# Optimization experiments

Hardware: AMD Instinct MI355X
Metric: run time of the kernel (lower is better)

Reference implementation:

```python
import jax, jax.numpy as jnp
import numpy as np

B, T, D, H, E, K = 4, 2048, 1024, 2048, 8, 2
LN_EPS = 1e-5


def setup_inputs() -> dict:
    key = jax.random.key(0)
    ks = jax.random.split(key, 5)
    sc = 0.02  # init scale for weights
    return {
        "x": jax.random.normal(ks[0], (B, T, D), dtype=jnp.float32),
        "gate_W": jax.random.normal(ks[1], (D, E), dtype=jnp.float32) * sc,
        "gate_b": jnp.zeros((E,), dtype=jnp.float32),
        "W1": jax.random.normal(ks[2], (E, D, H), dtype=jnp.float32) * sc,
        "b1": jnp.zeros((E, H), dtype=jnp.float32),
        "W2": jax.random.normal(ks[3], (E, H, D), dtype=jnp.float32) * sc,
        "b2": jnp.zeros((E, D), dtype=jnp.float32),
        "ln_gamma": jnp.ones((D,), dtype=jnp.float32),
        "ln_beta": jnp.zeros((D,), dtype=jnp.float32),
    }


def reference(x, gate_W, gate_b, W1, b1, W2, b2, ln_gamma, ln_beta):
    b, t, d = x.shape
    tokens = x.reshape(b * t, d)                      # [N, D]
    n = tokens.shape[0]

    # --- noisy top-k router (eval mode: no noise) ---
    logits = tokens @ gate_W + gate_b                 # [N, E]
    topk_val, topk_idx = jax.lax.top_k(logits, K)     # [N, K]
    topk_prob = jax.nn.softmax(topk_val, axis=-1)
    gates = jnp.zeros_like(logits).at[jnp.arange(n)[:, None], topk_idx].set(topk_prob)  # [N, E]

    # --- experts: dense-equivalent of gather-MLP-scatter (gates are 0 for unselected) ---
    h = jax.nn.gelu(jnp.einsum('nd,edh->enh', tokens, W1) + b1[:, None, :], approximate=False)  # [E,N,H]
    y = jnp.einsum('enh,ehd->end', h, W2) + b2[:, None, :]                                      # [E,N,D]
    out = jnp.einsum('ne,end->nd', gates, y).reshape(b, t, d)

    # --- residual + layernorm ---
    z = out + x
    mu = jnp.mean(z, axis=-1, keepdims=True)
    var = jnp.var(z, axis=-1, keepdims=True)
    out = (z - mu) * jax.lax.rsqrt(var + LN_EPS) * ln_gamma + ln_beta

    # --- aux losses ---
    route_probs = jax.nn.softmax(logits, axis=-1)     # [N, E]
    importance = route_probs.mean(axis=0)             # [E]
    load = (gates > 0).astype(jnp.float32).mean(axis=0)  # [E]
    balance_loss = E * jnp.sum(importance * load)
    eps = 1e-8
    entropy = -(route_probs * jnp.log(route_probs + eps)).sum(axis=-1).mean()
    utilization_entropy = -(load * jnp.log(load + eps)).sum()
    return out, balance_loss, entropy, utilization_entropy, load, importance
```

## Files before the change

kernel.cpp:

```cpp
#include <hip/hip_runtime.h>
#include <math.h>

#define N_TOK 8192
#define DIM   1024
#define HID   2048
#define NE    8
#define NPAIR (N_TOK * 2)
#define CAPP  (NPAIR + NE * 128)
#define TAIL  (N_TOK * DIM)

typedef __bf16 bf16x8_t __attribute__((ext_vector_type(8)));
typedef float  f32x4_t  __attribute__((ext_vector_type(4)));

__device__ __forceinline__ unsigned short f2bf(float f) {
  union { float f; unsigned u; } v; v.f = f;
  unsigned r = v.u + 0x7fffu + ((v.u >> 16) & 1u);
  return (unsigned short)(r >> 16);
}

__device__ __forceinline__ float bf2f(unsigned short h) {
  union { unsigned u; float f; } v; v.u = ((unsigned)h) << 16;
  return v.f;
}

__device__ __forceinline__ float gelu_exact(float v) {
  return 0.5f * v * (1.f + erff(v * 0.70710678118654752440f));
}

__device__ __forceinline__ void load16_lds(const void* g, void* l) {
  __builtin_amdgcn_global_load_lds(
      (const __attribute__((address_space(1))) unsigned int*)g,
      (__attribute__((address_space(3))) unsigned int*)l, 16, 0, 0);
}


template<int KD, int RR>
__global__ __launch_bounds__(256) void w_to_frag(const float* __restrict__ src,
                                                 unsigned short* __restrict__ dst) {
  constexpr int KD32 = KD / 32;
  int z = blockIdx.z;
  int cl = blockIdx.x * 4 + (threadIdx.x >> 6);
  int lane = threadIdx.x & 63, m16 = lane & 15, q = lane >> 4;
  int rblk = cl / KD32, kblk = cl % KD32;
  int r = rblk * 16 + m16;
  int kb = kblk * 32 + q * 8;
  const float* s = src + (size_t)z * KD * RR + (size_t)kb * RR + r;
  unsigned short t[8];
  #pragma unroll
  for (int j = 0; j < 8; ++j) t[j] = f2bf(s[(size_t)j * RR]);
  *(uint4*)(dst + (size_t)z * KD * RR + (size_t)cl * 512 + lane * 8) = *(uint4*)t;
}

#define R_BLOCKS 128
#define R_TPW    (N_TOK / (R_BLOCKS * 4))
__global__ __launch_bounds__(256) void router_kernel(
    const float* __restrict__ x, const float* __restrict__ gW, const float* __restrict__ gb,
    int* __restrict__ tok_e, float* __restrict__ tok_g,
    int* __restrict__ cnt, float* __restrict__ imp, float* __restrict__ ent_sum) {
  __shared__ int s_cnt[NE];
  __shared__ float s_imp[NE];
  __shared__ float s_ent;
  int tid = threadIdx.x;
  if (tid < NE) { s_cnt[tid] = 0; s_imp[tid] = 0.f; }
  if (tid == 0) s_ent = 0.f;
  __syncthreads();
  int wid = tid >> 6, lane = tid & 63;
  int t0 = (blockIdx.x * 4 + wid) * R_TPW;
  float imp_loc[8] = {0.f, 0.f, 0.f, 0.f, 0.f, 0.f, 0.f, 0.f};
  float ent_loc = 0.f;
  for (int t = 0; t < R_TPW; ++t) {
    int n = t0 + t;
    const float* xr = x + (size_t)n * DIM;
    float p[8] = {0.f, 0.f, 0.f, 0.f, 0.f, 0.f, 0.f, 0.f};
    #pragma unroll
    for (int it = 0; it < DIM / 64; ++it) {
      int d = lane + (it << 6);
      float xv = xr[d];
      const float4* g4 = (const float4*)(gW + (size_t)d * NE);
      float4 a = g4[0], b = g4[1];
      p[0] += xv * a.x; p[1] += xv * a.y; p[2] += xv * a.z; p[3] += xv * a.w;
      p[4] += xv * b.x; p[5] += xv * b.y; p[6] += xv * b.z; p[7] += xv * b.w;
    }
    #pragma unroll
    for (int e = 0; e < 8; ++e)
      for (int o = 32; o > 0; o >>= 1) p[e] += __shfl_down(p[e], o, 64);
    if (lane == 0) {
      float lg[8];
      #pragma unroll
      for (int e = 0; e < 8; ++e) lg[e] = p[e] + gb[e];
      int i0 = 0;
      #pragma unroll
      for (int e = 1; e < 8; ++e) if (lg[e] > lg[i0]) i0 = e;
      int i1 = (i0 == 0) ? 1 : 0;
      #pragma unroll
      for (int e = 0; e < 8; ++e) if (e != i0 && lg[e] > lg[i1]) i1 = e;
      float d1 = expf(lg[i1] - lg[i0]);
      float g0 = 1.f / (1.f + d1);
      float g1 = d1 * g0;
      tok_e[2 * n] = i0; tok_e[2 * n + 1] = i1;
      tok_g[2 * n] = g0; tok_g[2 * n + 1] = g1;
      atomicAdd(&s_cnt[i0], 1);
      atomicAdd(&s_cnt[i1], 1);
      float mx = lg[i0], s = 0.f, pe[8];
      #pragma unroll
      for (int e = 0; e < 8; ++e) { pe[e] = expf(lg[e] - mx); s += pe[e]; }
      float inv = 1.f / s;
      #pragma unroll
      for (int e = 0; e < 8; ++e) {
        float pr = pe[e] * inv;
        imp_loc[e] += pr;
        ent_loc -= pr * logf(pr + 1e-8f);
      }
    }
  }
  if (lane == 0) {
    #pragma unroll
    for (int e = 0; e < 8; ++e) atomicAdd(&s_imp[e], imp_loc[e]);
    atomicAdd(&s_ent, ent_loc);
  }
  __syncthreads();
  const float invN = 1.f / (float)N_TOK;
  if (tid < NE) {
    atomicAdd(&cnt[tid], s_cnt[tid]);
    atomicAdd(&imp[tid], s_imp[tid] * invN);
  }
  if (tid == NE) atomicAdd(ent_sum, s_ent * invN);
}

__global__ void finalize_kernel(const int* __restrict__ cnt, int* __restrict__ poffs,
                                int* __restrict__ cursor, const float* __restrict__ imp,
                                const float* __restrict__ ent_sum, float* __restrict__ out_tail) {
  if (threadIdx.x == 0) {
    int off = 0; float bal = 0.f, util = 0.f;
    for (int e = 0; e < NE; ++e) {
      poffs[e] = off; cursor[e] = off;
      off += ((cnt[e] + 127) >> 7) << 7;
      float ld = (float)cnt[e] * (1.f / (float)N_TOK);
      float im = imp[e];
      out_tail[3 + e] = ld;
      out_tail[11 + e] = im;
      bal += im * ld;
      util -= ld * logf(ld + 1e-8f);
    }
    poffs[NE] = off;
    out_tail[0] = (float)NE * bal;
    out_tail[1] = *ent_sum;
    out_tail[2] = util;
  }
}

__global__ __launch_bounds__(256) void scatter_kernel(
    const int* __restrict__ tok_e, const float* __restrict__ tok_g,
    int* __restrict__ cursor, int* __restrict__ row_token, float* __restrict__ row_gate,
    int* __restrict__ pair_slot) {
  __shared__ int s_cnt[NE], s_base[NE], s_rank[NE];
  int tid = threadIdx.x;
  if (tid < NE) { s_cnt[tid] = 0; s_rank[tid] = 0; }
  __syncthreads();
  int n = blockIdx.x * 256 + tid;
  int e0 = tok_e[2 * n], e1 = tok_e[2 * n + 1];
  atomicAdd(&s_cnt[e0], 1);
  atomicAdd(&s_cnt[e1], 1);
  __syncthreads();
  if (tid < NE) s_base[tid] = atomicAdd(&cursor[tid], s_cnt[tid]);
  __syncthreads();
  int r0 = atomicAdd(&s_rank[e0], 1);
  int s0 = s_base[e0] + r0;
  row_token[s0] = n; row_gate[s0] = tok_g[2 * n]; pair_slot[2 * n] = s0;
  int r1 = atomicAdd(&s_rank[e1], 1);
  int s1 = s_base[e1] + r1;
  row_token[s1] = n; row_gate[s1] = tok_g[2 * n + 1]; pair_slot[2 * n + 1] = s1;
}

__global__ __launch_bounds__(256) void gather_a1(
    const float* __restrict__ x, const int* __restrict__ row_token,
    const int* __restrict__ cnt, const int* __restrict__ poffs,
    unsigned short* __restrict__ Ab1) {
  int e = blockIdx.z;
  int base = poffs[e];
  int pcnt = poffs[e + 1] - base;
  int nch = (pcnt >> 4) * 32;
  int cl = blockIdx.x * 4 + (threadIdx.x >> 6);
  if (cl >= nch) return;
  int lane = threadIdx.x & 63, m16 = lane & 15, q = lane >> 4;
  int rblk = cl >> 5, kblk = cl & 31;
  int sl = rblk * 16 + m16;
  int slot = base + sl;
  int tok = (sl < cnt[e]) ? row_token[slot] : 0;
  int k = kblk * 32 + q * 8;
  const float4* sp = (const float4*)(x + (size_t)tok * DIM + k);
  float4 v0 = sp[0], v1 = sp[1];
  unsigned short t[8] = {f2bf(v0.x), f2bf(v0.y), f2bf(v0.z), f2bf(v0.w),
                         f2bf(v1.x), f2bf(v1.y), f2bf(v1.z), f2bf(v1.w)};
  *(uint4*)(Ab1 + ((size_t)(slot >> 4) * 32 + kblk) * 512 + lane * 8) = *(uint4*)t;
}

__global__ __launch_bounds__(256, 4) void expert_gemm1(
    const unsigned short* __restrict__ Ab1,
    const unsigned short* __restrict__ W1f,
    const float* __restrict__ b1,
    const int* __restrict__ poffs,
    unsigned short* __restrict__ He) {
  __shared__ __align__(16) unsigned short As[8192], Bs[8192];
  int e = blockIdx.z;
  int base = poffs[e];
  int pcnt = poffs[e + 1] - base;
  int row0 = blockIdx.x * 128;
  if (row0 >= pcnt) return;
  int col0 = blockIdx.y * 128;
  int tid = threadIdx.x, wid = tid >> 6, lane = tid & 63;
  int m16 = lane & 15, q = lane >> 4;
  int wr = (wid & 1) << 6, wc = (wid >> 1) << 6;
  const unsigned short* Ag = Ab1 + ((size_t)(((base + row0) >> 4) + wid * 2) * 32) * 512 + lane * 8;
  const unsigned short* Bg = W1f + (size_t)e * HID * DIM
                           + ((size_t)((col0 >> 4) + wid * 2) * 32) * 512 + lane * 8;
  unsigned short* lA = As + wid * 4 * 512;
  unsigned short* lB = Bs + wid * 4 * 512;
  f32x4_t zero4 = {0.f, 0.f, 0.f, 0.f};
  f32x4_t acc[4][4];
  #pragma unroll
  for (int i = 0; i < 4; ++i)
    #pragma unroll
    for (int j = 0; j < 4; ++j) acc[i][j] = zero4;
  int ra = wr >> 4, rc = wc >> 4;
  for (int k0 = 0; k0 < DIM; k0 += 64) {
    int kc = (k0 >> 5) * 512;
    load16_lds(Ag + kc,                  lA);
    load16_lds(Ag + kc + 512,            lA + 512);
    load16_lds(Ag + kc + 32 * 512,       lA + 1024);
    load16_lds(Ag + kc + 32 * 512 + 512, lA + 1536);
    load16_lds(Bg + kc,                  lB);
    load16_lds(Bg + kc + 512,            lB + 512);
    load16_lds(Bg + kc + 32 * 512,       lB + 1024);
    load16_lds(Bg + kc + 32 * 512 + 512, lB + 1536);
    __syncthreads();
    #pragma unroll
    for (int ks = 0; ks < 2; ++ks) {
      bf16x8_t a[4], b[4];
      #pragma unroll
      for (int i = 0; i < 4; ++i) {
        a[i] = *(const bf16x8_t*)&As[((ra + i) * 2 + ks) * 512 + lane * 8];
        b[i] = *(const bf16x8_t*)&Bs[((rc + i) * 2 + ks) * 512 + lane * 8];
      }
      #pragma unroll
      for (int i = 0; i < 4; ++i)
        #pragma unroll
        for (int j = 0; j < 4; ++j)
          acc[i][j] = __builtin_amdgcn_mfma_f32_16x16x32_bf16(a[i], b[j], acc[i][j], 0, 0, 0);
    }
    __syncthreads();
  }
  const float* b1e = b1 + (size_t)e * HID;
  int sb = (base + row0) >> 4;
  #pragma unroll
  for (int i = 0; i < 4; ++i) {
    size_t sblk = (size_t)(sb + ra + i);
    #pragma unroll
    for (int rr = 0; rr < 4; ++rr) {
      int s15 = q * 4 + rr;
      #pragma unroll
      for (int j = 0; j < 4; ++j) {
        int col = col0 + wc + j * 16 + m16;
        float v = acc[i][j][rr] + b1e[col];
        size_t off = (sblk * 64 + (col >> 5)) * 512 + (((col >> 3) & 3) * 16 + s15) * 8 + (col & 7);
        He[off] = f2bf(gelu_exact(v));
      }
    }
  }
}

__global__ __launch_bounds__(256, 4) void expert_gemm2(
    const unsigned short* __restrict__ He,
    const unsigned short* __restrict__ W2f,
    const int* __restrict__ poffs,
    unsigned short* __restrict__ yb) {
  __shared__ __align__(16) unsigned short As[8192], Bs[8192];
  int e = blockIdx.z;
  int base = poffs[e];
  int pcnt = poffs[e + 1] - base;
  int row0 = blockIdx.x * 128;
  if (row0 >= pcnt) return;
  int col0 = blockIdx.y * 128;
  int tid = threadIdx.x, wid = tid >> 6, lane = tid & 63;
  int m16 = lane & 15, q = lane >> 4;
  int wr = (wid & 1) << 6, wc = (wid >> 1) << 6;
  const unsigned short* Ag = He + ((size_t)(((base + row0) >> 4) + wid * 2) * 64) * 512 + lane * 8;
  const unsigned short* Bg = W2f + (size_t)e * DIM * HID
                           + ((size_t)((col0 >> 4) + wid * 2) * 64) * 512 + lane * 8;
  unsigned short* lA = As + wid * 4 * 512;
  unsigned short* lB = Bs + wid * 4 * 512;
  f32x4_t zero4 = {0.f, 0.f, 0.f, 0.f};
  f32x4_t acc[4][4];
  #pragma unroll
  for (int i = 0; i < 4; ++i)
    #pragma unroll
    for (int j = 0; j < 4; ++j) acc[i][j] = zero4;
  int ra = wr >> 4, rc = wc >> 4;
  for (int k0 = 0; k0 < HID; k0 += 64) {
    int kc = (k0 >> 5) * 512;
    load16_lds(Ag + kc,                  lA);
    load16_lds(Ag + kc + 512,            lA + 512);
    load16_lds(Ag + kc + 64 * 512,       lA + 1024);
    load16_lds(Ag + kc + 64 * 512 + 512, lA + 1536);
    load16_lds(Bg + kc,                  lB);
    load16_lds(Bg + kc + 512,            lB + 512);
    load16_lds(Bg + kc + 64 * 512,       lB + 1024);
    load16_lds(Bg + kc + 64 * 512 + 512, lB + 1536);
    __syncthreads();
    #pragma unroll
    for (int ks = 0; ks < 2; ++ks) {
      bf16x8_t a[4], b[4];
      #pragma unroll
      for (int i = 0; i < 4; ++i) {
        a[i] = *(const bf16x8_t*)&As[((ra + i) * 2 + ks) * 512 + lane * 8];
        b[i] = *(const bf16x8_t*)&Bs[((rc + i) * 2 + ks) * 512 + lane * 8];
      }
      #pragma unroll
      for (int i = 0; i < 4; ++i)
        #pragma unroll
        for (int j = 0; j < 4; ++j)
          acc[i][j] = __builtin_amdgcn_mfma_f32_16x16x32_bf16(a[i], b[j], acc[i][j], 0, 0, 0);
    }
    __syncthreads();
  }
  #pragma unroll
  for (int i = 0; i < 4; ++i) {
    #pragma unroll
    for (int rr = 0; rr < 4; ++rr) {
      size_t slot = (size_t)(base + row0 + wr + i * 16 + q * 4 + rr);
      #pragma unroll
      for (int j = 0; j < 4; ++j) {
        int col = col0 + wc + j * 16 + m16;
        yb[slot * DIM + col] = f2bf(acc[i][j][rr]);
      }
    }
  }
}

__global__ __launch_bounds__(256) void ln_kernel(
    const float* __restrict__ x, const unsigned short* __restrict__ yb,
    const int* __restrict__ tok_e, const float* __restrict__ tok_g,
    const int* __restrict__ pair_slot, const float* __restrict__ b2,
    const float* __restrict__ gamma, const float* __restrict__ beta,
    float* __restrict__ out) {
  int n = blockIdx.x, tid = threadIdx.x;
  int e0 = tok_e[2 * n], e1 = tok_e[2 * n + 1];
  float g0 = tok_g[2 * n], g1 = tok_g[2 * n + 1];
  size_t s0 = (size_t)pair_slot[2 * n], s1 = (size_t)pair_slot[2 * n + 1];
  const float* xr = x + (size_t)n * DIM;
  const unsigned short* y0 = yb + s0 * DIM;
  const unsigned short* y1 = yb + s1 * DIM;
  const float* b2e0 = b2 + (size_t)e0 * DIM;
  const float* b2e1 = b2 + (size_t)e1 * DIM;
  float z[4], s = 0.f, s2 = 0.f;
  #pragma unroll
  for (int jj = 0; jj < 4; ++jj) {
    int d = tid + (jj << 8);
    float v = xr[d] + g0 * (bf2f(y0[d]) + b2e0[d]) + g1 * (bf2f(y1[d]) + b2e1[d]);
    z[jj] = v; s += v; s2 += v * v;
  }
  for (int o = 32; o > 0; o >>= 1) { s += __shfl_down(s, o, 64); s2 += __shfl_down(s2, o, 64); }
  __shared__ float rs[4], rs2[4];
  int wid = tid >> 6, lane = tid & 63;
  if (lane == 0) { rs[wid] = s; rs2[wid] = s2; }
  __syncthreads();
  float ts = rs[0] + rs[1] + rs[2] + rs[3];
  float ts2 = rs2[0] + rs2[1] + rs2[2] + rs2[3];
  float mu = ts * (1.f / DIM);
  float var = ts2 * (1.f / DIM) - mu * mu;
  float rstd = rsqrtf(var + 1e-5f);
  float* orow = out + (size_t)n * DIM;
  #pragma unroll
  for (int jj = 0; jj < 4; ++jj) {
    int d = tid + (jj << 8);
    orow[d] = (z[jj] - mu) * rstd * gamma[d] + beta[d];
  }
}

extern "C" void kernel_launch(void* const* d_in, const int* in_sizes, int n_in,
                              void* d_out, int out_size, void* d_ws, size_t ws_size,
                              hipStream_t stream) {
  const float* x     = (const float*)d_in[0];
  const float* gW    = (const float*)d_in[1];
  const float* gb    = (const float*)d_in[2];
  const float* W1    = (const float*)d_in[3];
  const float* b1    = (const float*)d_in[4];
  const float* W2    = (const float*)d_in[5];
  const float* b2    = (const float*)d_in[6];
  const float* gamma = (const float*)d_in[7];
  const float* beta  = (const float*)d_in[8];
  float* out = (float*)d_out;

  char* w = (char*)d_ws;
  unsigned short* W1f = (unsigned short*)w; w += (size_t)NE * HID * DIM * 2;
  unsigned short* W2f = (unsigned short*)w; w += (size_t)NE * DIM * HID * 2;
  unsigned short* He  = (unsigned short*)w; w += (size_t)CAPP * HID * 2;
  unsigned short* AbY = (unsigned short*)w; w += (size_t)CAPP * DIM * 2;
  int*   row_token    = (int*)w;            w += (size_t)CAPP * 4;
  float* row_gate     = (float*)w;          w += (size_t)CAPP * 4;
  int*   tok_e        = (int*)w;            w += (size_t)NPAIR * 4;
  float* tok_g        = (float*)w;          w += (size_t)NPAIR * 4;
  int*   pair_slot    = (int*)w;            w += (size_t)NPAIR * 4;
  float* imp          = (float*)w;
  float* ent_sum      = imp + 8;
  int*   cntp         = (int*)(imp + 16);
  int*   cursor       = cntp + 8;
  int*   poffs        = cursor + 8;

  unsigned short* Ab1 = AbY;
  unsigned short* yb  = AbY;

  hipMemsetAsync(imp, 0, 256, stream);

  w_to_frag<DIM, HID><<<dim3(1024, 1, NE), 256, 0, stream>>>(W1, W1f);
  w_to_frag<HID, DIM><<<dim3(1024, 1, NE), 256, 0, stream>>>(W2, W2f);
  router_kernel<<<R_BLOCKS, 256, 0, stream>>>(x, gW, gb, tok_e, tok_g, cntp, imp, ent_sum);
  finalize_kernel<<<1, 64, 0, stream>>>(cntp, poffs, cursor, imp, ent_sum, out + TAIL);
  scatter_kernel<<<N_TOK / 256, 256, 0, stream>>>(tok_e, tok_g, cursor, row_token, row_gate, pair_slot);
  gather_a1<<<dim3(4096, 1, NE), 256, 0, stream>>>(x, row_token, cntp, poffs, Ab1);
  expert_gemm1<<<dim3(64, HID / 128, NE), 256, 0, stream>>>(Ab1, W1f, b1, poffs, He);
  expert_gemm2<<<dim3(64, DIM / 128, NE), 256, 0, stream>>>(He, W2f, poffs, yb);
  ln_kernel<<<N_TOK, 256, 0, stream>>>(x, yb, tok_e, tok_g, pair_slot, b2, gamma, beta, out);
}
```

Before: 529.0 us.

## Double-buffer LDS tiles in both expert GEMMs to overlap loads with MFMA

Both expert GEMM kernels now use two LDS buffers per operand. The loop issues the global-to-LDS load for the next K tile while MFMA runs on the current one, which halves the barriers per tile and hides load latency. The doubled LDS footprint (64 KB per block) forces the launch bound down from 4 to 2 blocks per CU, cutting occupancy and the latency hiding that came from running more blocks at once.

```diff
diff --git a/kernel.cpp b/kernel.cpp
--- a/kernel.cpp
+++ b/kernel.cpp
@@ -195,13 +195,14 @@
   *(uint4*)(Ab1 + ((size_t)(slot >> 4) * 32 + kblk) * 512 + lane * 8) = *(uint4*)t;
 }
 
-__global__ __launch_bounds__(256, 4) void expert_gemm1(
+__global__ __launch_bounds__(256, 2) void expert_gemm1(
     const unsigned short* __restrict__ Ab1,
     const unsigned short* __restrict__ W1f,
     const float* __restrict__ b1,
     const int* __restrict__ poffs,
     unsigned short* __restrict__ He) {
-  __shared__ __align__(16) unsigned short As[8192], Bs[8192];
+  __shared__ __align__(16) unsigned short As0[8192], Bs0[8192];
+  __shared__ __align__(16) unsigned short As1[8192], Bs1[8192];
   int e = blockIdx.z;
   int base = poffs[e];
   int pcnt = poffs[e + 1] - base;
@@ -214,8 +215,6 @@
   const unsigned short* Ag = Ab1 + ((size_t)(((base + row0) >> 4) + wid * 2) * 32) * 512 + lane * 8;
   const unsigned short* Bg = W1f + (size_t)e * HID * DIM
                            + ((size_t)((col0 >> 4) + wid * 2) * 32) * 512 + lane * 8;
-  unsigned short* lA = As + wid * 4 * 512;
-  unsigned short* lB = Bs + wid * 4 * 512;
   f32x4_t zero4 = {0.f, 0.f, 0.f, 0.f};
   f32x4_t acc[4][4];
   #pragma unroll
@@ -223,8 +222,11 @@
     #pragma unroll
     for (int j = 0; j < 4; ++j) acc[i][j] = zero4;
   int ra = wr >> 4, rc = wc >> 4;
-  for (int k0 = 0; k0 < DIM; k0 += 64) {
-    int kc = (k0 >> 5) * 512;
+
+  auto stage = [&](unsigned short* SA, unsigned short* SB, int t) {
+    int kc = t << 10;
+    unsigned short* lA = SA + (wid << 11);
+    unsigned short* lB = SB + (wid << 11);
     load16_lds(Ag + kc,                  lA);
     load16_lds(Ag + kc + 512,            lA + 512);
     load16_lds(Ag + kc + 32 * 512,       lA + 1024);
@@ -233,14 +235,15 @@
     load16_lds(Bg + kc + 512,            lB + 512);
     load16_lds(Bg + kc + 32 * 512,       lB + 1024);
     load16_lds(Bg + kc + 32 * 512 + 512, lB + 1536);
-    __syncthreads();
+  };
+  auto compute = [&](const unsigned short* SA, const unsigned short* SB) {
     #pragma unroll
     for (int ks = 0; ks < 2; ++ks) {
       bf16x8_t a[4], b[4];
       #pragma unroll
       for (int i = 0; i < 4; ++i) {
-        a[i] = *(const bf16x8_t*)&As[((ra + i) * 2 + ks) * 512 + lane * 8];
-        b[i] = *(const bf16x8_t*)&Bs[((rc + i) * 2 + ks) * 512 + lane * 8];
+        a[i] = *(const bf16x8_t*)&SA[((ra + i) * 2 + ks) * 512 + lane * 8];
+        b[i] = *(const bf16x8_t*)&SB[((rc + i) * 2 + ks) * 512 + lane * 8];
       }
       #pragma unroll
       for (int i = 0; i < 4; ++i)
@@ -248,8 +251,20 @@
         for (int j = 0; j < 4; ++j)
           acc[i][j] = __builtin_amdgcn_mfma_f32_16x16x32_bf16(a[i], b[j], acc[i][j], 0, 0, 0);
     }
+  };
+
+  constexpr int NT = DIM / 64;
+  stage(As0, Bs0, 0);
+  __syncthreads();
+  for (int t = 0; t < NT; t += 2) {
+    stage(As1, Bs1, t + 1);
+    compute(As0, Bs0);
     __syncthreads();
-  }
+    if (t + 2 < NT) stage(As0, Bs0, t + 2);
+    compute(As1, Bs1);
+    __syncthreads();
+  }
+
   const float* b1e = b1 + (size_t)e * HID;
   int sb = (base + row0) >> 4;
   #pragma unroll
@@ -269,12 +284,13 @@
   }
 }
 
-__global__ __launch_bounds__(256, 4) void expert_gemm2(
+__global__ __launch_bounds__(256, 2) void expert_gemm2(
     const unsigned short* __restrict__ He,
     const unsigned short* __restrict__ W2f,
     const int* __restrict__ poffs,
     unsigned short* __restrict__ yb) {
-  __shared__ __align__(16) unsigned short As[8192], Bs[8192];
+  __shared__ __align__(16) unsigned short As0[8192], Bs0[8192];
+  __shared__ __align__(16) unsigned short As1[8192], Bs1[8192];
   int e = blockIdx.z;
   int base = poffs[e];
   int pcnt = poffs[e + 1] - base;
@@ -287,8 +303,6 @@
   const unsigned short* Ag = He + ((size_t)(((base + row0) >> 4) + wid * 2) * 64) * 512 + lane * 8;
   const unsigned short* Bg = W2f + (size_t)e * DIM * HID
                            + ((size_t)((col0 >> 4) + wid * 2) * 64) * 512 + lane * 8;
-  unsigned short* lA = As + wid * 4 * 512;
-  unsigned short* lB = Bs + wid * 4 * 512;
   f32x4_t zero4 = {0.f, 0.f, 0.f, 0.f};
   f32x4_t acc[4][4];
   #pragma unroll
@@ -296,8 +310,11 @@
     #pragma unroll
     for (int j = 0; j < 4; ++j) acc[i][j] = zero4;
   int ra = wr >> 4, rc = wc >> 4;
-  for (int k0 = 0; k0 < HID; k0 += 64) {
-    int kc = (k0 >> 5) * 512;
+
+  auto stage = [&](unsigned short* SA, unsigned short* SB, int t) {
+    int kc = t << 10;
+    unsigned short* lA = SA + (wid << 11);
+    unsigned short* lB = SB + (wid << 11);
     load16_lds(Ag + kc,                  lA);
     load16_lds(Ag + kc + 512,            lA + 512);
     load16_lds(Ag + kc + 64 * 512,       lA + 1024);
@@ -306,14 +323,15 @@
     load16_lds(Bg + kc + 512,            lB + 512);
     load16_lds(Bg + kc + 64 * 512,       lB + 1024);
     load16_lds(Bg + kc + 64 * 512 + 512, lB + 1536);
-    __syncthreads();
+  };
+  auto compute = [&](const unsigned short* SA, const unsigned short* SB) {
     #pragma unroll
     for (int ks = 0; ks < 2; ++ks) {
       bf16x8_t a[4], b[4];
       #pragma unroll
       for (int i = 0; i < 4; ++i) {
-        a[i] = *(const bf16x8_t*)&As[((ra + i) * 2 + ks) * 512 + lane * 8];
-        b[i] = *(const bf16x8_t*)&Bs[((rc + i) * 2 + ks) * 512 + lane * 8];
+        a[i] = *(const bf16x8_t*)&SA[((ra + i) * 2 + ks) * 512 + lane * 8];
+        b[i] = *(const bf16x8_t*)&SB[((rc + i) * 2 + ks) * 512 + lane * 8];
       }
       #pragma unroll
       for (int i = 0; i < 4; ++i)
@@ -321,8 +339,20 @@
         for (int j = 0; j < 4; ++j)
           acc[i][j] = __builtin_amdgcn_mfma_f32_16x16x32_bf16(a[i], b[j], acc[i][j], 0, 0, 0);
     }
+  };
+
+  constexpr int NT = HID / 64;
+  stage(As0, Bs0, 0);
+  __syncthreads();
+  for (int t = 0; t < NT; t += 2) {
+    stage(As1, Bs1, t + 1);
+    compute(As0, Bs0);
     __syncthreads();
-  }
+    if (t + 2 < NT) stage(As0, Bs0, t + 2);
+    compute(As1, Bs1);
+    __syncthreads();
+  }
+
   #pragma unroll
   for (int i = 0; i < 4; ++i) {
     #pragma unroll
```

After: 589.0 us. 11.3% more time.

## Convert expert GEMMs to persistent grid over flattened compacted tile list

Applied to the files above, without the earlier changes.

Replaces the 3D grid (64 row tiles × column tiles × experts, with most blocks exiting early) by a fixed 1024-block persistent grid. Each block walks a flattened list of real 128x128 tiles across all experts and finds the owning expert by scanning the padded offsets. This removes launch and early-exit overhead from empty blocks and balances work across CUs. It relies on each expert's padded segment being aligned to 128 rows so that no tile straddles two experts.

```diff
diff --git a/kernel.cpp b/kernel.cpp
--- a/kernel.cpp
+++ b/kernel.cpp
@@ -195,6 +195,8 @@
   *(uint4*)(Ab1 + ((size_t)(slot >> 4) * 32 + kblk) * 512 + lane * 8) = *(uint4*)t;
 }
 
+#define GEMM_BLOCKS 1024
+
 __global__ __launch_bounds__(256, 4) void expert_gemm1(
     const unsigned short* __restrict__ Ab1,
     const unsigned short* __restrict__ W1f,
@@ -202,68 +204,76 @@
     const int* __restrict__ poffs,
     unsigned short* __restrict__ He) {
   __shared__ __align__(16) unsigned short As[8192], Bs[8192];
-  int e = blockIdx.z;
-  int base = poffs[e];
-  int pcnt = poffs[e + 1] - base;
-  int row0 = blockIdx.x * 128;
-  if (row0 >= pcnt) return;
-  int col0 = blockIdx.y * 128;
+  __shared__ int s_po[NE + 1];
   int tid = threadIdx.x, wid = tid >> 6, lane = tid & 63;
+  if (tid <= NE) s_po[tid] = poffs[tid];
+  __syncthreads();
+  int nt = (s_po[NE] >> 7) << 4;
   int m16 = lane & 15, q = lane >> 4;
   int wr = (wid & 1) << 6, wc = (wid >> 1) << 6;
-  const unsigned short* Ag = Ab1 + ((size_t)(((base + row0) >> 4) + wid * 2) * 32) * 512 + lane * 8;
-  const unsigned short* Bg = W1f + (size_t)e * HID * DIM
-                           + ((size_t)((col0 >> 4) + wid * 2) * 32) * 512 + lane * 8;
+  int ra = wr >> 4, rc = wc >> 4;
   unsigned short* lA = As + wid * 4 * 512;
   unsigned short* lB = Bs + wid * 4 * 512;
   f32x4_t zero4 = {0.f, 0.f, 0.f, 0.f};
-  f32x4_t acc[4][4];
-  #pragma unroll
-  for (int i = 0; i < 4; ++i)
-    #pragma unroll
-    for (int j = 0; j < 4; ++j) acc[i][j] = zero4;
-  int ra = wr >> 4, rc = wc >> 4;
-  for (int k0 = 0; k0 < DIM; k0 += 64) {
-    int kc = (k0 >> 5) * 512;
-    load16_lds(Ag + kc,                  lA);
-    load16_lds(Ag + kc + 512,            lA + 512);
-    load16_lds(Ag + kc + 32 * 512,       lA + 1024);
-    load16_lds(Ag + kc + 32 * 512 + 512, lA + 1536);
-    load16_lds(Bg + kc,                  lB);
-    load16_lds(Bg + kc + 512,            lB + 512);
-    load16_lds(Bg + kc + 32 * 512,       lB + 1024);
-    load16_lds(Bg + kc + 32 * 512 + 512, lB + 1536);
-    __syncthreads();
-    #pragma unroll
-    for (int ks = 0; ks < 2; ++ks) {
-      bf16x8_t a[4], b[4];
-      #pragma unroll
-      for (int i = 0; i < 4; ++i) {
-        a[i] = *(const bf16x8_t*)&As[((ra + i) * 2 + ks) * 512 + lane * 8];
-        b[i] = *(const bf16x8_t*)&Bs[((rc + i) * 2 + ks) * 512 + lane * 8];
+
+  for (int tile = blockIdx.x; tile < nt; tile += GEMM_BLOCKS) {
+    int rt = tile >> 4, ct = tile & 15;
+    int row0 = rt << 7;
+    int col0 = ct << 7;
+    int e = 0;
+    while (e + 1 < NE && s_po[e + 1] <= row0) ++e;
+    const unsigned short* Ag = Ab1 + ((size_t)((rt << 3) + wid * 2) * 32) * 512 + lane * 8;
+    const unsigned short* Bg = W1f + (size_t)e * HID * DIM
+                             + ((size_t)((col0 >> 4) + wid * 2) * 32) * 512 + lane * 8;
+    f32x4_t acc[4][4];
+    #pragma unroll
+    for (int i = 0; i < 4; ++i)
+      #pragma unroll
+      for (int j = 0; j < 4; ++j) acc[i][j] = zero4;
+
+    for (int k0 = 0; k0 < DIM; k0 += 64) {
+      int kc = (k0 >> 5) * 512;
+      load16_lds(Ag + kc,                  lA);
+      load16_lds(Ag + kc + 512,            lA + 512);
+      load16_lds(Ag + kc + 32 * 512,       lA + 1024);
+      load16_lds(Ag + kc + 32 * 512 + 512, lA + 1536);
+      load16_lds(Bg + kc,                  lB);
+      load16_lds(Bg + kc + 512,            lB + 512);
+      load16_lds(Bg + kc + 32 * 512,       lB + 1024);
+      load16_lds(Bg + kc + 32 * 512 + 512, lB + 1536);
+      __syncthreads();
+      #pragma unroll
+      for (int ks = 0; ks < 2; ++ks) {
+        bf16x8_t a[4], b[4];
+        #pragma unroll
+        for (int i = 0; i < 4; ++i) {
+          a[i] = *(const bf16x8_t*)&As[((ra + i) * 2 + ks) * 512 + lane * 8];
+          b[i] = *(const bf16x8_t*)&Bs[((rc + i) * 2 + ks) * 512 + lane * 8];
+        }
+        #pragma unroll
+        for (int i = 0; i < 4; ++i)
+          #pragma unroll
+          for (int j = 0; j < 4; ++j)
+            acc[i][j] = __builtin_amdgcn_mfma_f32_16x16x32_bf16(a[i], b[j], acc[i][j], 0, 0, 0);
       }
-      #pragma unroll
-      for (int i = 0; i < 4; ++i)
-        #pragma unroll
-        for (int j = 0; j < 4; ++j)
-          acc[i][j] = __builtin_amdgcn_mfma_f32_16x16x32_bf16(a[i], b[j], acc[i][j], 0, 0, 0);
-    }
-    __syncthreads();
-  }
-  const float* b1e = b1 + (size_t)e * HID;
-  int sb = (base + row0) >> 4;
-  #pragma unroll
-  for (int i = 0; i < 4; ++i) {
-    size_t sblk = (size_t)(sb + ra + i);
-    #pragma unroll
-    for (int rr = 0; rr < 4; ++rr) {
-      int s15 = q * 4 + rr;
-      #pragma unroll
-      for (int j = 0; j < 4; ++j) {
-        int col = col0 + wc + j * 16 + m16;
-        float v = acc[i][j][rr] + b1e[col];
-        size_t off = (sblk * 64 + (col >> 5)) * 512 + (((col >> 3) & 3) * 16 + s15) * 8 + (col & 7);
-        He[off] = f2bf(gelu_exact(v));
+      __syncthreads();
+    }
+
+    const float* b1e = b1 + (size_t)e * HID;
+    int sb = rt << 3;
+    #pragma unroll
+    for (int i = 0; i < 4; ++i) {
+      size_t sblk = (size_t)(sb + ra + i);
+      #pragma unroll
+      for (int rr = 0; rr < 4; ++rr) {
+        int s15 = q * 4 + rr;
+        #pragma unroll
+        for (int j = 0; j < 4; ++j) {
+          int col = col0 + wc + j * 16 + m16;
+          float v = acc[i][j][rr] + b1e[col];
+          size_t off = (sblk * 64 + (col >> 5)) * 512 + (((col >> 3) & 3) * 16 + s15) * 8 + (col & 7);
+          He[off] = f2bf(gelu_exact(v));
+        }
       }
     }
   }
@@ -275,63 +285,71 @@
     const int* __restrict__ poffs,
     unsigned short* __restrict__ yb) {
   __shared__ __align__(16) unsigned short As[8192], Bs[8192];
-  int e = blockIdx.z;
-  int base = poffs[e];
-  int pcnt = poffs[e + 1] - base;
-  int row0 = blockIdx.x * 128;
-  if (row0 >= pcnt) return;
-  int col0 = blockIdx.y * 128;
+  __shared__ int s_po[NE + 1];
   int tid = threadIdx.x, wid = tid >> 6, lane = tid & 63;
+  if (tid <= NE) s_po[tid] = poffs[tid];
+  __syncthreads();
+  int nt = (s_po[NE] >> 7) << 3;
   int m16 = lane & 15, q = lane >> 4;
   int wr = (wid & 1) << 6, wc = (wid >> 1) << 6;
-  const unsigned short* Ag = He + ((size_t)(((base + row0) >> 4) + wid * 2) * 64) * 512 + lane * 8;
-  const unsigned short* Bg = W2f + (size_t)e * DIM * HID
-                           + ((size_t)((col0 >> 4) + wid * 2) * 64) * 512 + lane * 8;
+  int ra = wr >> 4, rc = wc >> 4;
   unsigned short* lA = As + wid * 4 * 512;
   unsigned short* lB = Bs + wid * 4 * 512;
   f32x4_t zero4 = {0.f, 0.f, 0.f, 0.f};
-  f32x4_t acc[4][4];
-  #pragma unroll
-  for (int i = 0; i < 4; ++i)
-    #pragma unroll
-    for (int j = 0; j < 4; ++j) acc[i][j] = zero4;
-  int ra = wr >> 4, rc = wc >> 4;
-  for (int k0 = 0; k0 < HID; k0 += 64) {
-    int kc = (k0 >> 5) * 512;
-    load16_lds(Ag + kc,                  lA);
-    load16_lds(Ag + kc + 512,            lA + 512);
-    load16_lds(Ag + kc + 64 * 512,       lA + 1024);
-    load16_lds(Ag + kc + 64 * 512 + 512, lA + 1536);
-    load16_lds(Bg + kc,                  lB);
-    load16_lds(Bg + kc + 512,            lB + 512);
-    load16_lds(Bg + kc + 64 * 512,       lB + 1024);
-    load16_lds(Bg + kc + 64 * 512 + 512, lB + 1536);
-    __syncthreads();
-    #pragma unroll
-    for (int ks = 0; ks < 2; ++ks) {
-      bf16x8_t a[4], b[4];
-      #pragma unroll
-      for (int i = 0; i < 4; ++i) {
-        a[i] = *(const bf16x8_t*)&As[((ra + i) * 2 + ks) * 512 + lane * 8];
-        b[i] = *(const bf16x8_t*)&Bs[((rc + i) * 2 + ks) * 512 + lane * 8];
+
+  for (int tile = blockIdx.x; tile < nt; tile += GEMM_BLOCKS) {
+    int rt = tile >> 3, ct = tile & 7;
+    int row0 = rt << 7;
+    int col0 = ct << 7;
+    int e = 0;
+    while (e + 1 < NE && s_po[e + 1] <= row0) ++e;
+    const unsigned short* Ag = He + ((size_t)((rt << 3) + wid * 2) * 64) * 512 + lane * 8;
+    const unsigned short* Bg = W2f + (size_t)e * DIM * HID
+                             + ((size_t)((col0 >> 4) + wid * 2) * 64) * 512 + lane * 8;
+    f32x4_t acc[4][4];
+    #pragma unroll
+    for (int i = 0; i < 4; ++i)
+      #pragma unroll
+      for (int j = 0; j < 4; ++j) acc[i][j] = zero4;
+
+    for (int k0 = 0; k0 < HID; k0 += 64) {
+      int kc = (k0 >> 5) * 512;
+      load16_lds(Ag + kc,                  lA);
+      load16_lds(Ag + kc + 512,            lA + 512);
+      load16_lds(Ag + kc + 64 * 512,       lA + 1024);
+      load16_lds(Ag + kc + 64 * 512 + 512, lA + 1536);
+      load16_lds(Bg + kc,                  lB);
+      load16_lds(Bg + kc + 512,            lB + 512);
+      load16_lds(Bg + kc + 64 * 512,       lB + 1024);
+      load16_lds(Bg + kc + 64 * 512 + 512, lB + 1536);
+      __syncthreads();
+      #pragma unroll
+      for (int ks = 0; ks < 2; ++ks) {
+        bf16x8_t a[4], b[4];
+        #pragma unroll
+        for (int i = 0; i < 4; ++i) {
+          a[i] = *(const bf16x8_t*)&As[((ra + i) * 2 + ks) * 512 + lane * 8];
+          b[i] = *(const bf16x8_t*)&Bs[((rc + i) * 2 + ks) * 512 + lane * 8];
+        }
+        #pragma unroll
+        for (int i = 0; i < 4; ++i)
+          #pragma unroll
+          for (int j = 0; j < 4; ++j)
+            acc[i][j] = __builtin_amdgcn_mfma_f32_16x16x32_bf16(a[i], b[j], acc[i][j], 0, 0, 0);
       }
-      #pragma unroll
-      for (int i = 0; i < 4; ++i)
-        #pragma unroll
-        for (int j = 0; j < 4; ++j)
-          acc[i][j] = __builtin_amdgcn_mfma_f32_16x16x32_bf16(a[i], b[j], acc[i][j], 0, 0, 0);
-    }
-    __syncthreads();
-  }
-  #pragma unroll
-  for (int i = 0; i < 4; ++i) {
-    #pragma unroll
-    for (int rr = 0; rr < 4; ++rr) {
-      size_t slot = (size_t)(base + row0 + wr + i * 16 + q * 4 + rr);
-      #pragma unroll
-      for (int j = 0; j < 4; ++j) {
-        int col = col0 + wc + j * 16 + m16;
-        yb[slot * DIM + col] = f2bf(acc[i][j][rr]);
+      __syncthreads();
+    }
+
+    #pragma unroll
+    for (int i = 0; i < 4; ++i) {
+      #pragma unroll
+      for (int rr = 0; rr < 4; ++rr) {
+        size_t slot = (size_t)(row0 + wr + i * 16 + q * 4 + rr);
+        #pragma unroll
+        for (int j = 0; j < 4; ++j) {
+          int col = col0 + wc + j * 16 + m16;
+          yb[slot * DIM + col] = f2bf(acc[i][j][rr]);
+        }
       }
     }
   }
@@ -418,7 +436,7 @@
   finalize_kernel<<<1, 64, 0, stream>>>(cntp, poffs, cursor, imp, ent_sum, out + TAIL);
   scatter_kernel<<<N_TOK / 256, 256, 0, stream>>>(tok_e, tok_g, cursor, row_token, row_gate, pair_slot);
   gather_a1<<<dim3(4096, 1, NE), 256, 0, stream>>>(x, row_token, cntp, poffs, Ab1);
-  expert_gemm1<<<dim3(64, HID / 128, NE), 256, 0, stream>>>(Ab1, W1f, b1, poffs, He);
-  expert_gemm2<<<dim3(64, DIM / 128, NE), 256, 0, stream>>>(He, W2f, poffs, yb);
+  expert_gemm1<<<GEMM_BLOCKS, 256, 0, stream>>>(Ab1, W1f, b1, poffs, He);
+  expert_gemm2<<<GEMM_BLOCKS, 256, 0, stream>>>(He, W2f, poffs, yb);
   ln_kernel<<<N_TOK, 256, 0, stream>>>(x, yb, tok_e, tok_g, pair_slot, b2, gamma, beta, out);
 }
```

Result: faster. 506.2 us (-4.3%).
